# Kernel optimization log

Hardware: AMD Instinct MI355X
Metric: run time of the kernel (lower is better)

Reference implementation:

```python
import jax, jax.numpy as jnp
import numpy as np

# Complete binary tree: node 0 is the root, node i's parent is (i-1)//2.
# adjacency[i, j] = 1 iff j is the parent of i (matches _parent_indices/_child_indices).
N_LEVELS = 11
N_LABELS = 2 ** N_LEVELS - 1  # 2047
N_CLASSES = 2
BATCH = 2048


def _tree_structure():
    # levels[t]: node ids at tree level t (root level 0)
    levels = [np.arange(2 ** t - 1, 2 ** (t + 1) - 1) for t in range(N_LEVELS)]
    parent = np.zeros(N_LABELS, dtype=np.int64)
    parent[1:] = (np.arange(1, N_LABELS) - 1) // 2
    return levels, parent


def _propagate(emissions, transitions, edge_layers):
    """Belief-propagation sweep. edge_layers is a list (per depth, in order)
    of (src, dst) numpy index arrays: each src node sends a message to dst.
    Message: m[b, c_dst, dst] += logsumexp_{c_src}(emissions[b,c_src,src]
              + messages[b,c_src,src] + transitions[dst, src, c_dst, c_src]).
    Identical math to (Batched)MessagePassing.forward, expressed per edge.
    """
    messages = jnp.zeros_like(emissions)
    for src, dst in edge_layers:
        e = emissions[:, :, src] + messages[:, :, src]           # [B, Cs, E]
        t = transitions[dst, src]                                 # [E, Cd, Cs]
        # elem[b, cd, e, cs] = e[b, cs, e] + t[e, cd, cs]
        elem = e.transpose(0, 2, 1)[:, None, :, :] + t.transpose(1, 0, 2)[None]
        contrib = jax.nn.logsumexp(elem, axis=-1)                 # [B, Cd, E]
        messages = messages.at[:, :, dst].add(contrib)
    return messages


def setup_inputs() -> dict:
    key = jax.random.key(0)
    k1, k2 = jax.random.split(key)
    emissions = jax.random.normal(k1, (BATCH, N_CLASSES, N_LABELS), dtype=jnp.float32)
    transitions = jax.random.normal(k2, (N_LABELS, N_LABELS, N_CLASSES, N_CLASSES), dtype=jnp.float32)
    return {"emissions": emissions, "transitions": transitions}


def reference(emissions, transitions):
    levels, parent = _tree_structure()
    # upward (alphas): leaves -> root, successor = parent
    up_edges = [(levels[t], parent[levels[t]]) for t in range(N_LEVELS - 1, 0, -1)]
    # downward (betas): root -> leaves, successor = child
    down_edges = [(parent[levels[t]], levels[t]) for t in range(1, N_LEVELS)]
    alphas = _propagate(emissions, transitions, up_edges)
    betas = _propagate(emissions, transitions, down_edges)
    scores = emissions + alphas + betas                           # [B, C, L]
    # normalize over classes per label -> marginal log-probabilities
    return scores - jax.nn.logsumexp(scores, axis=1, keepdims=True)
```

## Files before the change

kernel.cpp:

```cpp
#include <hip/hip_runtime.h>


#define L 2047
#define NSLOT 49
#define PK_ELEMS (2 * NSLOT * 64)

typedef float __attribute__((ext_vector_type(4), aligned(4))) uf4;
typedef float __attribute__((ext_vector_type(2), aligned(4))) uf2;

__device__ __forceinline__ float lse2(float x, float y) {
    float m = fmaxf(x, y);
    return m + __logf(1.0f + __expf(fminf(x, y) - m));
}

__device__ __forceinline__ void up_pair(float c00, float c01, float c10, float c11,
                                        float4 tA, float4 tB, float em0, float em1,
                                        float& o0, float& o1) {
    o0 = em0 + lse2(c00 + tA.x, c01 + tA.y) + lse2(c10 + tB.x, c11 + tB.y);
    o1 = em1 + lse2(c00 + tA.z, c01 + tA.w) + lse2(c10 + tB.z, c11 + tB.w);
}

__device__ __forceinline__ void slot_decode(int r, int s, int l, int& dst, int& src) {
    const int n7 = 127 + 64 * r + l;
    if (s < 8)       { int k = s >> 1;      dst = 4*n7 + 3 + k;         src = 2*dst + 1 + (s & 1); }
    else if (s < 12) { int j = (s - 8) >> 1;dst = 2*n7 + 1 + j;         src = 2*dst + 1 + (s & 1); }
    else if (s < 14) {                      dst = n7;                   src = 2*n7 + 1 + (s - 12); }
    else if (s < 26) { int d = (s - 14) >> 1; dst = ((n7+1) >> (d+1)) - 1; src = 2*dst + 1 + (s & 1); }
    else if (s < 28) {                      dst = 0;                    src = 1 + (s - 26); }
    else if (s < 34) { int t = s - 27;      dst = ((n7+1) >> (7-t)) - 1; src = (dst - 1) >> 1; }
    else if (s < 35) {                      dst = n7;                   src = (n7 - 1) >> 1; }
    else if (s < 37) {                      dst = 2*n7 + 1 + (s - 35);  src = n7; }
    else if (s < 41) {                      dst = 4*n7 + 3 + (s - 37);  src = (dst - 1) >> 1; }
    else             {                      dst = 8*n7 + 7 + (s - 41);  src = (dst - 1) >> 1; }
}

__global__ void pack_kernel(const float4* __restrict__ tr4, float4* __restrict__ pk) {
    int idx = blockIdx.x * 256 + threadIdx.x;
    if (idx >= PK_ELEMS) return;
    int r = idx / (NSLOT * 64);
    int rem = idx - r * (NSLOT * 64);
    int s = rem >> 6, l = rem & 63;
    int d_, c_; slot_decode(r, s, l, d_, c_);
    pk[idx] = tr4[d_ * L + c_];
}

template <bool UPK>
__global__ __launch_bounds__(128, 4) void treecrf_main(
    const float* __restrict__ emissions,
    const float4* __restrict__ pk,
    const float4* __restrict__ tr4,
    float* __restrict__ out)
{
    __shared__ float sh[4];
    const int tid = threadIdx.x;
    const int l = tid & 63;
    const int r = tid >> 6;
    const int b = blockIdx.x;
    const float* __restrict__ e0 = emissions + (size_t)b * (2 * L);
    const float* __restrict__ e1 = e0 + L;
    float* __restrict__ o0 = out + (size_t)b * (2 * L);
    float* __restrict__ o1 = o0 + L;

    auto FL = [&](int s) -> float4 {
        if (UPK) return pk[((r * NSLOT + s) << 6) + l];
        int d_, c_; slot_decode(r, s, l, d_, c_);
        return tr4[d_ * L + c_];
    };

    float el0[8], el1[8];
    {
        const uf4* p0 = (const uf4*)(e0 + 1023 + 512*r + 8*l);
        const uf4* p1 = (const uf4*)(e1 + 1023 + 512*r + 8*l);
        uf4 a = p0[0], c = p0[1], d = p1[0], e = p1[1];
        el0[0]=a.x; el0[1]=a.y; el0[2]=a.z; el0[3]=a.w;
        el0[4]=c.x; el0[5]=c.y; el0[6]=c.z; el0[7]=c.w;
        el1[0]=d.x; el1[1]=d.y; el1[2]=d.z; el1[3]=d.w;
        el1[4]=e.x; el1[5]=e.y; el1[6]=e.z; el1[7]=e.w;
    }
    float em9_0[4], em9_1[4], em8_0[2], em8_1[2], em7_0, em7_1;
    {
        uf4 a = *(const uf4*)(e0 + 511 + 256*r + 4*l);
        uf4 c = *(const uf4*)(e1 + 511 + 256*r + 4*l);
        em9_0[0]=a.x; em9_0[1]=a.y; em9_0[2]=a.z; em9_0[3]=a.w;
        em9_1[0]=c.x; em9_1[1]=c.y; em9_1[2]=c.z; em9_1[3]=c.w;
        uf2 g = *(const uf2*)(e0 + 255 + 128*r + 2*l);
        uf2 h = *(const uf2*)(e1 + 255 + 128*r + 2*l);
        em8_0[0]=g.x; em8_0[1]=g.y; em8_1[0]=h.x; em8_1[1]=h.y;
        em7_0 = e0[127 + 64*r + l]; em7_1 = e1[127 + 64*r + l];
    }
    float Ea0[7], Ea1[7];
    Ea0[0] = e0[0]; Ea1[0] = e1[0];
    #pragma unroll
    for (int t = 1; t <= 6; ++t) {
        const int n = ((128 + 64*r + l) >> (7 - t)) - 1;
        Ea0[t] = e0[n]; Ea1[t] = e1[n];
    }

    float A9_0[4], A9_1[4];
    #pragma unroll
    for (int k = 0; k < 4; ++k)
        up_pair(el0[2*k], el1[2*k], el0[2*k+1], el1[2*k+1], FL(2*k), FL(2*k+1),
                em9_0[k], em9_1[k], A9_0[k], A9_1[k]);
    float A8_0[2], A8_1[2];
    #pragma unroll
    for (int j = 0; j < 2; ++j)
        up_pair(A9_0[2*j], A9_1[2*j], A9_0[2*j+1], A9_1[2*j+1], FL(8+2*j), FL(9+2*j),
                em8_0[j], em8_1[j], A8_0[j], A8_1[j]);
    float A7_0, A7_1;
    up_pair(A8_0[0], A8_1[0], A8_0[1], A8_1[1], FL(12), FL(13), em7_0, em7_1, A7_0, A7_1);

    float cur0 = A7_0, cur1 = A7_1;
    float Aa0[7], Aa1[7];
    #pragma unroll
    for (int d = 0; d < 6; ++d) {
        const int t = 6 - d;
        float p0v = __shfl_xor(cur0, 1 << d);
        float p1v = __shfl_xor(cur1, 1 << d);
        bool isL = ((l >> d) & 1) == 0;
        float Lc0 = isL ? cur0 : p0v, Lc1 = isL ? cur1 : p1v;
        float Rc0 = isL ? p0v : cur0, Rc1 = isL ? p1v : cur1;
        up_pair(Lc0, Lc1, Rc0, Rc1, FL(14 + 2*d), FL(15 + 2*d),
                Ea0[t], Ea1[t], cur0, cur1);
        Aa0[t] = cur0; Aa1[t] = cur1;
    }

    if (l == 0) { sh[2*r] = cur0; sh[2*r + 1] = cur1; }
    __syncthreads();
    {
        float a1_0 = sh[0], a1_1 = sh[1], a2_0 = sh[2], a2_1 = sh[3];
        float4 t1 = FL(26), t2 = FL(27);
        float AR0 = Ea0[0] + lse2(a1_0 + t1.x, a1_1 + t1.y)
                           + lse2(a2_0 + t2.x, a2_1 + t2.y);
        float AR1 = Ea1[0] + lse2(a1_0 + t1.z, a1_1 + t1.w)
                           + lse2(a2_0 + t2.z, a2_1 + t2.w);
        if (r == 0 && l == 0) {
            float m = lse2(AR0, AR1);
            o0[0] = AR0 - m; o1[0] = AR1 - m;
        }
    }

    float D0 = Ea0[0], D1 = Ea1[0];
    #pragma unroll
    for (int t = 1; t <= 6; ++t) {
        float4 td = FL(27 + t);
        float b0 = lse2(D0 + td.x, D1 + td.y);
        float b1 = lse2(D0 + td.z, D1 + td.w);
        float s0 = Aa0[t] + b0, s1 = Aa1[t] + b1, m = lse2(s0, s1);
        if ((l & ((1 << (7 - t)) - 1)) == 0) {
            const int n = ((128 + 64*r + l) >> (7 - t)) - 1;
            o0[n] = s0 - m; o1[n] = s1 - m;
        }
        D0 = Ea0[t] + b0; D1 = Ea1[t] + b1;
    }

    {
        float4 td = FL(34);
        float b0 = lse2(D0 + td.x, D1 + td.y);
        float b1 = lse2(D0 + td.z, D1 + td.w);
        float s0 = A7_0 + b0, s1 = A7_1 + b1, m = lse2(s0, s1);
        o0[127 + 64*r + l] = s0 - m; o1[127 + 64*r + l] = s1 - m;
        D0 = em7_0 + b0; D1 = em7_1 + b1;
    }

    float D8_0[2], D8_1[2];
    {
        float w0[2], w1[2];
        #pragma unroll
        for (int j = 0; j < 2; ++j) {
            float4 td = FL(35 + j);
            float b0 = lse2(D0 + td.x, D1 + td.y);
            float b1 = lse2(D0 + td.z, D1 + td.w);
            float s0 = A8_0[j] + b0, s1 = A8_1[j] + b1, m = lse2(s0, s1);
            w0[j] = s0 - m; w1[j] = s1 - m;
            D8_0[j] = em8_0[j] + b0; D8_1[j] = em8_1[j] + b1;
        }
        *(uf2*)(o0 + 255 + 128*r + 2*l) = uf2{w0[0], w0[1]};
        *(uf2*)(o1 + 255 + 128*r + 2*l) = uf2{w1[0], w1[1]};
    }

    float D9_0[4], D9_1[4];
    {
        float w0[4], w1[4];
        #pragma unroll
        for (int k = 0; k < 4; ++k) {
            float4 td = FL(37 + k);
            float b0 = lse2(D8_0[k>>1] + td.x, D8_1[k>>1] + td.y);
            float b1 = lse2(D8_0[k>>1] + td.z, D8_1[k>>1] + td.w);
            float s0 = A9_0[k] + b0, s1 = A9_1[k] + b1, m = lse2(s0, s1);
            w0[k] = s0 - m; w1[k] = s1 - m;
            D9_0[k] = em9_0[k] + b0; D9_1[k] = em9_1[k] + b1;
        }
        *(uf4*)(o0 + 511 + 256*r + 4*l) = uf4{w0[0], w0[1], w0[2], w0[3]};
        *(uf4*)(o1 + 511 + 256*r + 4*l) = uf4{w1[0], w1[1], w1[2], w1[3]};
    }

    {
        float w0[8], w1[8];
        #pragma unroll
        for (int m2 = 0; m2 < 8; ++m2) {
            float4 td = FL(41 + m2);
            float b0 = lse2(D9_0[m2>>1] + td.x, D9_1[m2>>1] + td.y);
            float b1 = lse2(D9_0[m2>>1] + td.z, D9_1[m2>>1] + td.w);
            float s0 = el0[m2] + b0, s1 = el1[m2] + b1, m = lse2(s0, s1);
            w0[m2] = s0 - m; w1[m2] = s1 - m;
        }
        uf4* q0 = (uf4*)(o0 + 1023 + 512*r + 8*l);
        uf4* q1 = (uf4*)(o1 + 1023 + 512*r + 8*l);
        q0[0] = uf4{w0[0], w0[1], w0[2], w0[3]}; q0[1] = uf4{w0[4], w0[5], w0[6], w0[7]};
        q1[0] = uf4{w1[0], w1[1], w1[2], w1[3]}; q1[1] = uf4{w1[4], w1[5], w1[6], w1[7]};
    }
}

extern "C" void kernel_launch(void* const* d_in, const int* in_sizes, int n_in,
                              void* d_out, int out_size, void* d_ws, size_t ws_size,
                              hipStream_t stream) {
    const float* emissions = (const float*)d_in[0];
    const float4* tr4 = (const float4*)d_in[1];
    float* out = (float*)d_out;

    const size_t packed_bytes = (size_t)PK_ELEMS * sizeof(float4);
    const bool use_ws = (ws_size >= packed_bytes) && (d_ws != nullptr);
    if (use_ws) {
        float4* pk = (float4*)d_ws;
        pack_kernel<<<(PK_ELEMS + 255) / 256, 256, 0, stream>>>(tr4, pk);
        treecrf_main<true><<<2048, 128, 0, stream>>>(emissions, pk, tr4, out);
    } else {
        treecrf_main<false><<<2048, 128, 0, stream>>>(emissions, nullptr, tr4, out);
    }
}
```

Baseline: 133.5 us.

## Process two batch rows per thread to reuse transition loads

Restructures the main kernel so each thread computes two batch elements, with 256-thread blocks covering four batch rows and a grid of 512 blocks. Each packed transition float4 is loaded once and applied to both rows, halving transition-load traffic per row and adding ILP. The cost is roughly doubled register state per thread, which can reduce occupancy, and fewer, larger blocks.

Result: slower. 136.6 us (+2.3%).

```diff
diff --git a/kernel.cpp b/kernel.cpp
--- a/kernel.cpp
+++ b/kernel.cpp
@@ -45,21 +45,28 @@
 }
 
 template <bool UPK>
-__global__ __launch_bounds__(128, 4) void treecrf_main(
+__global__ __launch_bounds__(256, 2) void treecrf_main(
     const float* __restrict__ emissions,
     const float4* __restrict__ pk,
     const float4* __restrict__ tr4,
     float* __restrict__ out)
 {
-    __shared__ float sh[4];
+    __shared__ float sh[16];
     const int tid = threadIdx.x;
     const int l = tid & 63;
-    const int r = tid >> 6;
-    const int b = blockIdx.x;
-    const float* __restrict__ e0 = emissions + (size_t)b * (2 * L);
-    const float* __restrict__ e1 = e0 + L;
-    float* __restrict__ o0 = out + (size_t)b * (2 * L);
-    float* __restrict__ o1 = o0 + L;
+    const int w = tid >> 6;
+    const int r = w >> 1;
+    const int p = w & 1;
+    const int bb = blockIdx.x * 4 + p * 2;
+
+    const float* e0[2]; const float* e1[2]; float* o0[2]; float* o1[2];
+    #pragma unroll
+    for (int q = 0; q < 2; ++q) {
+        e0[q] = emissions + (size_t)(bb + q) * (2 * L);
+        e1[q] = e0[q] + L;
+        o0[q] = out + (size_t)(bb + q) * (2 * L);
+        o1[q] = o0[q] + L;
+    }
 
     auto FL = [&](int s) -> float4 {
         if (UPK) return pk[((r * NSLOT + s) << 6) + l];
@@ -67,147 +74,201 @@
         return tr4[d_ * L + c_];
     };
 
-    float el0[8], el1[8];
-    {
-        const uf4* p0 = (const uf4*)(e0 + 1023 + 512*r + 8*l);
-        const uf4* p1 = (const uf4*)(e1 + 1023 + 512*r + 8*l);
-        uf4 a = p0[0], c = p0[1], d = p1[0], e = p1[1];
-        el0[0]=a.x; el0[1]=a.y; el0[2]=a.z; el0[3]=a.w;
-        el0[4]=c.x; el0[5]=c.y; el0[6]=c.z; el0[7]=c.w;
-        el1[0]=d.x; el1[1]=d.y; el1[2]=d.z; el1[3]=d.w;
-        el1[4]=e.x; el1[5]=e.y; el1[6]=e.z; el1[7]=e.w;
-    }
-    float em9_0[4], em9_1[4], em8_0[2], em8_1[2], em7_0, em7_1;
-    {
-        uf4 a = *(const uf4*)(e0 + 511 + 256*r + 4*l);
-        uf4 c = *(const uf4*)(e1 + 511 + 256*r + 4*l);
-        em9_0[0]=a.x; em9_0[1]=a.y; em9_0[2]=a.z; em9_0[3]=a.w;
-        em9_1[0]=c.x; em9_1[1]=c.y; em9_1[2]=c.z; em9_1[3]=c.w;
-        uf2 g = *(const uf2*)(e0 + 255 + 128*r + 2*l);
-        uf2 h = *(const uf2*)(e1 + 255 + 128*r + 2*l);
-        em8_0[0]=g.x; em8_0[1]=g.y; em8_1[0]=h.x; em8_1[1]=h.y;
-        em7_0 = e0[127 + 64*r + l]; em7_1 = e1[127 + 64*r + l];
-    }
-    float Ea0[7], Ea1[7];
-    Ea0[0] = e0[0]; Ea1[0] = e1[0];
-    #pragma unroll
-    for (int t = 1; t <= 6; ++t) {
-        const int n = ((128 + 64*r + l) >> (7 - t)) - 1;
-        Ea0[t] = e0[n]; Ea1[t] = e1[n];
-    }
-
-    float A9_0[4], A9_1[4];
-    #pragma unroll
-    for (int k = 0; k < 4; ++k)
-        up_pair(el0[2*k], el1[2*k], el0[2*k+1], el1[2*k+1], FL(2*k), FL(2*k+1),
-                em9_0[k], em9_1[k], A9_0[k], A9_1[k]);
-    float A8_0[2], A8_1[2];
-    #pragma unroll
-    for (int j = 0; j < 2; ++j)
-        up_pair(A9_0[2*j], A9_1[2*j], A9_0[2*j+1], A9_1[2*j+1], FL(8+2*j), FL(9+2*j),
-                em8_0[j], em8_1[j], A8_0[j], A8_1[j]);
-    float A7_0, A7_1;
-    up_pair(A8_0[0], A8_1[0], A8_0[1], A8_1[1], FL(12), FL(13), em7_0, em7_1, A7_0, A7_1);
-
-    float cur0 = A7_0, cur1 = A7_1;
-    float Aa0[7], Aa1[7];
+    float el0[2][8], el1[2][8];
+    float em9_0[2][4], em9_1[2][4], em8_0[2][2], em8_1[2][2], em7_0[2], em7_1[2];
+    float Ea0[2][7], Ea1[2][7];
+    #pragma unroll
+    for (int q = 0; q < 2; ++q) {
+        const uf4* pA = (const uf4*)(e0[q] + 1023 + 512*r + 8*l);
+        const uf4* pB = (const uf4*)(e1[q] + 1023 + 512*r + 8*l);
+        uf4 a = pA[0], b2 = pA[1], c = pB[0], d = pB[1];
+        el0[q][0]=a.x;  el0[q][1]=a.y;  el0[q][2]=a.z;  el0[q][3]=a.w;
+        el0[q][4]=b2.x; el0[q][5]=b2.y; el0[q][6]=b2.z; el0[q][7]=b2.w;
+        el1[q][0]=c.x;  el1[q][1]=c.y;  el1[q][2]=c.z;  el1[q][3]=c.w;
+        el1[q][4]=d.x;  el1[q][5]=d.y;  el1[q][6]=d.z;  el1[q][7]=d.w;
+        uf4 a9 = *(const uf4*)(e0[q] + 511 + 256*r + 4*l);
+        uf4 c9 = *(const uf4*)(e1[q] + 511 + 256*r + 4*l);
+        em9_0[q][0]=a9.x; em9_0[q][1]=a9.y; em9_0[q][2]=a9.z; em9_0[q][3]=a9.w;
+        em9_1[q][0]=c9.x; em9_1[q][1]=c9.y; em9_1[q][2]=c9.z; em9_1[q][3]=c9.w;
+        uf2 g = *(const uf2*)(e0[q] + 255 + 128*r + 2*l);
+        uf2 h = *(const uf2*)(e1[q] + 255 + 128*r + 2*l);
+        em8_0[q][0]=g.x; em8_0[q][1]=g.y; em8_1[q][0]=h.x; em8_1[q][1]=h.y;
+        em7_0[q] = e0[q][127 + 64*r + l]; em7_1[q] = e1[q][127 + 64*r + l];
+        Ea0[q][0] = e0[q][0]; Ea1[q][0] = e1[q][0];
+        #pragma unroll
+        for (int t = 1; t <= 6; ++t) {
+            const int n = ((128 + 64*r + l) >> (7 - t)) - 1;
+            Ea0[q][t] = e0[q][n]; Ea1[q][t] = e1[q][n];
+        }
+    }
+
+    float A9_0[2][4], A9_1[2][4];
+    #pragma unroll
+    for (int k = 0; k < 4; ++k) {
+        float4 tA = FL(2*k), tB = FL(2*k + 1);
+        #pragma unroll
+        for (int q = 0; q < 2; ++q)
+            up_pair(el0[q][2*k], el1[q][2*k], el0[q][2*k+1], el1[q][2*k+1], tA, tB,
+                    em9_0[q][k], em9_1[q][k], A9_0[q][k], A9_1[q][k]);
+    }
+    float A8_0[2][2], A8_1[2][2];
+    #pragma unroll
+    for (int j = 0; j < 2; ++j) {
+        float4 tA = FL(8 + 2*j), tB = FL(9 + 2*j);
+        #pragma unroll
+        for (int q = 0; q < 2; ++q)
+            up_pair(A9_0[q][2*j], A9_1[q][2*j], A9_0[q][2*j+1], A9_1[q][2*j+1], tA, tB,
+                    em8_0[q][j], em8_1[q][j], A8_0[q][j], A8_1[q][j]);
+    }
+    float A7_0[2], A7_1[2];
+    {
+        float4 tA = FL(12), tB = FL(13);
+        #pragma unroll
+        for (int q = 0; q < 2; ++q)
+            up_pair(A8_0[q][0], A8_1[q][0], A8_0[q][1], A8_1[q][1], tA, tB,
+                    em7_0[q], em7_1[q], A7_0[q], A7_1[q]);
+    }
+
+    float cur0[2] = {A7_0[0], A7_0[1]}, cur1[2] = {A7_1[0], A7_1[1]};
+    float Aa0[2][7], Aa1[2][7];
     #pragma unroll
     for (int d = 0; d < 6; ++d) {
         const int t = 6 - d;
-        float p0v = __shfl_xor(cur0, 1 << d);
-        float p1v = __shfl_xor(cur1, 1 << d);
+        float4 tL = FL(14 + 2*d), tR = FL(15 + 2*d);
         bool isL = ((l >> d) & 1) == 0;
-        float Lc0 = isL ? cur0 : p0v, Lc1 = isL ? cur1 : p1v;
-        float Rc0 = isL ? p0v : cur0, Rc1 = isL ? p1v : cur1;
-        up_pair(Lc0, Lc1, Rc0, Rc1, FL(14 + 2*d), FL(15 + 2*d),
-                Ea0[t], Ea1[t], cur0, cur1);
-        Aa0[t] = cur0; Aa1[t] = cur1;
-    }
-
-    if (l == 0) { sh[2*r] = cur0; sh[2*r + 1] = cur1; }
+        #pragma unroll
+        for (int q = 0; q < 2; ++q) {
+            float p0v = __shfl_xor(cur0[q], 1 << d);
+            float p1v = __shfl_xor(cur1[q], 1 << d);
+            float Lc0 = isL ? cur0[q] : p0v, Lc1 = isL ? cur1[q] : p1v;
+            float Rc0 = isL ? p0v : cur0[q], Rc1 = isL ? p1v : cur1[q];
+            up_pair(Lc0, Lc1, Rc0, Rc1, tL, tR, Ea0[q][t], Ea1[q][t],
+                    cur0[q], cur1[q]);
+            Aa0[q][t] = cur0[q]; Aa1[q][t] = cur1[q];
+        }
+    }
+
+    if (l == 0) {
+        #pragma unroll
+        for (int q = 0; q < 2; ++q) {
+            sh[p*8 + q*4 + r*2 + 0] = cur0[q];
+            sh[p*8 + q*4 + r*2 + 1] = cur1[q];
+        }
+    }
     __syncthreads();
     {
-        float a1_0 = sh[0], a1_1 = sh[1], a2_0 = sh[2], a2_1 = sh[3];
         float4 t1 = FL(26), t2 = FL(27);
-        float AR0 = Ea0[0] + lse2(a1_0 + t1.x, a1_1 + t1.y)
-                           + lse2(a2_0 + t2.x, a2_1 + t2.y);
-        float AR1 = Ea1[0] + lse2(a1_0 + t1.z, a1_1 + t1.w)
-                           + lse2(a2_0 + t2.z, a2_1 + t2.w);
         if (r == 0 && l == 0) {
-            float m = lse2(AR0, AR1);
-            o0[0] = AR0 - m; o1[0] = AR1 - m;
-        }
-    }
-
-    float D0 = Ea0[0], D1 = Ea1[0];
+            #pragma unroll
+            for (int q = 0; q < 2; ++q) {
+                float a1_0 = sh[p*8 + q*4 + 0], a1_1 = sh[p*8 + q*4 + 1];
+                float a2_0 = sh[p*8 + q*4 + 2], a2_1 = sh[p*8 + q*4 + 3];
+                float AR0 = Ea0[q][0] + lse2(a1_0 + t1.x, a1_1 + t1.y)
+                                      + lse2(a2_0 + t2.x, a2_1 + t2.y);
+                float AR1 = Ea1[q][0] + lse2(a1_0 + t1.z, a1_1 + t1.w)
+                                      + lse2(a2_0 + t2.z, a2_1 + t2.w);
+                float m = lse2(AR0, AR1);
+                o0[q][0] = AR0 - m; o1[q][0] = AR1 - m;
+            }
+        }
+    }
+
+    float D0[2], D1[2];
+    #pragma unroll
+    for (int q = 0; q < 2; ++q) { D0[q] = Ea0[q][0]; D1[q] = Ea1[q][0]; }
     #pragma unroll
     for (int t = 1; t <= 6; ++t) {
         float4 td = FL(27 + t);
-        float b0 = lse2(D0 + td.x, D1 + td.y);
-        float b1 = lse2(D0 + td.z, D1 + td.w);
-        float s0 = Aa0[t] + b0, s1 = Aa1[t] + b1, m = lse2(s0, s1);
-        if ((l & ((1 << (7 - t)) - 1)) == 0) {
-            const int n = ((128 + 64*r + l) >> (7 - t)) - 1;
-            o0[n] = s0 - m; o1[n] = s1 - m;
-        }
-        D0 = Ea0[t] + b0; D1 = Ea1[t] + b1;
+        const bool emit = (l & ((1 << (7 - t)) - 1)) == 0;
+        const int n = ((128 + 64*r + l) >> (7 - t)) - 1;
+        #pragma unroll
+        for (int q = 0; q < 2; ++q) {
+            float b0v = lse2(D0[q] + td.x, D1[q] + td.y);
+            float b1v = lse2(D0[q] + td.z, D1[q] + td.w);
+            float s0 = Aa0[q][t] + b0v, s1 = Aa1[q][t] + b1v, m = lse2(s0, s1);
+            if (emit) { o0[q][n] = s0 - m; o1[q][n] = s1 - m; }
+            D0[q] = Ea0[q][t] + b0v; D1[q] = Ea1[q][t] + b1v;
+        }
     }
 
     {
         float4 td = FL(34);
-        float b0 = lse2(D0 + td.x, D1 + td.y);
-        float b1 = lse2(D0 + td.z, D1 + td.w);
-        float s0 = A7_0 + b0, s1 = A7_1 + b1, m = lse2(s0, s1);
-        o0[127 + 64*r + l] = s0 - m; o1[127 + 64*r + l] = s1 - m;
-        D0 = em7_0 + b0; D1 = em7_1 + b1;
-    }
-
-    float D8_0[2], D8_1[2];
-    {
-        float w0[2], w1[2];
+        #pragma unroll
+        for (int q = 0; q < 2; ++q) {
+            float b0v = lse2(D0[q] + td.x, D1[q] + td.y);
+            float b1v = lse2(D0[q] + td.z, D1[q] + td.w);
+            float s0 = A7_0[q] + b0v, s1 = A7_1[q] + b1v, m = lse2(s0, s1);
+            o0[q][127 + 64*r + l] = s0 - m; o1[q][127 + 64*r + l] = s1 - m;
+            D0[q] = em7_0[q] + b0v; D1[q] = em7_1[q] + b1v;
+        }
+    }
+
+    float D8_0[2][2], D8_1[2][2];
+    {
+        float w0[2][2], w1[2][2];
         #pragma unroll
         for (int j = 0; j < 2; ++j) {
             float4 td = FL(35 + j);
-            float b0 = lse2(D0 + td.x, D1 + td.y);
-            float b1 = lse2(D0 + td.z, D1 + td.w);
-            float s0 = A8_0[j] + b0, s1 = A8_1[j] + b1, m = lse2(s0, s1);
-            w0[j] = s0 - m; w1[j] = s1 - m;
-            D8_0[j] = em8_0[j] + b0; D8_1[j] = em8_1[j] + b1;
-        }
-        *(uf2*)(o0 + 255 + 128*r + 2*l) = uf2{w0[0], w0[1]};
-        *(uf2*)(o1 + 255 + 128*r + 2*l) = uf2{w1[0], w1[1]};
-    }
-
-    float D9_0[4], D9_1[4];
-    {
-        float w0[4], w1[4];
+            #pragma unroll
+            for (int q = 0; q < 2; ++q) {
+                float b0v = lse2(D0[q] + td.x, D1[q] + td.y);
+                float b1v = lse2(D0[q] + td.z, D1[q] + td.w);
+                float s0 = A8_0[q][j] + b0v, s1 = A8_1[q][j] + b1v, m = lse2(s0, s1);
+                w0[q][j] = s0 - m; w1[q][j] = s1 - m;
+                D8_0[q][j] = em8_0[q][j] + b0v; D8_1[q][j] = em8_1[q][j] + b1v;
+            }
+        }
+        #pragma unroll
+        for (int q = 0; q < 2; ++q) {
+            *(uf2*)(o0[q] + 255 + 128*r + 2*l) = uf2{w0[q][0], w0[q][1]};
+            *(uf2*)(o1[q] + 255 + 128*r + 2*l) = uf2{w1[q][0], w1[q][1]};
+        }
+    }
+
+    float D9_0[2][4], D9_1[2][4];
+    {
+        float w0[2][4], w1[2][4];
         #pragma unroll
         for (int k = 0; k < 4; ++k) {
             float4 td = FL(37 + k);
-            float b0 = lse2(D8_0[k>>1] + td.x, D8_1[k>>1] + td.y);
-            float b1 = lse2(D8_0[k>>1] + td.z, D8_1[k>>1] + td.w);
-            float s0 = A9_0[k] + b0, s1 = A9_1[k] + b1, m = lse2(s0, s1);
-            w0[k] = s0 - m; w1[k] = s1 - m;
-            D9_0[k] = em9_0[k] + b0; D9_1[k] = em9_1[k] + b1;
-        }
-        *(uf4*)(o0 + 511 + 256*r + 4*l) = uf4{w0[0], w0[1], w0[2], w0[3]};
-        *(uf4*)(o1 + 511 + 256*r + 4*l) = uf4{w1[0], w1[1], w1[2], w1[3]};
-    }
-
-    {
-        float w0[8], w1[8];
+            #pragma unroll
+            for (int q = 0; q < 2; ++q) {
+                float b0v = lse2(D8_0[q][k>>1] + td.x, D8_1[q][k>>1] + td.y);
+                float b1v = lse2(D8_0[q][k>>1] + td.z, D8_1[q][k>>1] + td.w);
+                float s0 = A9_0[q][k] + b0v, s1 = A9_1[q][k] + b1v, m = lse2(s0, s1);
+                w0[q][k] = s0 - m; w1[q][k] = s1 - m;
+                D9_0[q][k] = em9_0[q][k] + b0v; D9_1[q][k] = em9_1[q][k] + b1v;
+            }
+        }
+        #pragma unroll
+        for (int q = 0; q < 2; ++q) {
+            *(uf4*)(o0[q] + 511 + 256*r + 4*l) = uf4{w0[q][0], w0[q][1], w0[q][2], w0[q][3]};
+            *(uf4*)(o1[q] + 511 + 256*r + 4*l) = uf4{w1[q][0], w1[q][1], w1[q][2], w1[q][3]};
+        }
+    }
+
+    {
+        float w0[2][8], w1[2][8];
         #pragma unroll
         for (int m2 = 0; m2 < 8; ++m2) {
             float4 td = FL(41 + m2);
-            float b0 = lse2(D9_0[m2>>1] + td.x, D9_1[m2>>1] + td.y);
-            float b1 = lse2(D9_0[m2>>1] + td.z, D9_1[m2>>1] + td.w);
-            float s0 = el0[m2] + b0, s1 = el1[m2] + b1, m = lse2(s0, s1);
-            w0[m2] = s0 - m; w1[m2] = s1 - m;
-        }
-        uf4* q0 = (uf4*)(o0 + 1023 + 512*r + 8*l);
-        uf4* q1 = (uf4*)(o1 + 1023 + 512*r + 8*l);
-        q0[0] = uf4{w0[0], w0[1], w0[2], w0[3]}; q0[1] = uf4{w0[4], w0[5], w0[6], w0[7]};
-        q1[0] = uf4{w1[0], w1[1], w1[2], w1[3]}; q1[1] = uf4{w1[4], w1[5], w1[6], w1[7]};
+            #pragma unroll
+            for (int q = 0; q < 2; ++q) {
+                float b0v = lse2(D9_0[q][m2>>1] + td.x, D9_1[q][m2>>1] + td.y);
+                float b1v = lse2(D9_0[q][m2>>1] + td.z, D9_1[q][m2>>1] + td.w);
+                float s0 = el0[q][m2] + b0v, s1 = el1[q][m2] + b1v, m = lse2(s0, s1);
+                w0[q][m2] = s0 - m; w1[q][m2] = s1 - m;
+            }
+        }
+        #pragma unroll
+        for (int q = 0; q < 2; ++q) {
+            uf4* q0 = (uf4*)(o0[q] + 1023 + 512*r + 8*l);
+            uf4* q1 = (uf4*)(o1[q] + 1023 + 512*r + 8*l);
+            q0[0] = uf4{w0[q][0], w0[q][1], w0[q][2], w0[q][3]};
+            q0[1] = uf4{w0[q][4], w0[q][5], w0[q][6], w0[q][7]};
+            q1[0] = uf4{w1[q][0], w1[q][1], w1[q][2], w1[q][3]};
+            q1[1] = uf4{w1[q][4], w1[q][5], w1[q][6], w1[q][7]};
+        }
     }
 }
 
@@ -223,8 +284,8 @@
     if (use_ws) {
         float4* pk = (float4*)d_ws;
         pack_kernel<<<(PK_ELEMS + 255) / 256, 256, 0, stream>>>(tr4, pk);
-        treecrf_main<true><<<2048, 128, 0, stream>>>(emissions, pk, tr4, out);
+        treecrf_main<true><<<512, 256, 0, stream>>>(emissions, pk, tr4, out);
     } else {
-        treecrf_main<false><<<2048, 128, 0, stream>>>(emissions, nullptr, tr4, out);
-    }
-}
+        treecrf_main<false><<<512, 256, 0, stream>>>(emissions, nullptr, tr4, out);
+    }
+}
```

## Precompute exp of transitions in pack step, use sum-product logsumexp

Applied to the files above, without the earlier changes.

The pack kernel now stores exp(transitions) instead of raw transitions. Upward and downward messages are computed as max plus log of an exp-weighted sum, which cuts the number of exp/log calls per edge (two exps and two logs for a pair instead of four of each). The root computation is also limited to a single thread. This trades some numerical range, since exp(t) is unguarded and products of the sums could under- or overflow, for fewer transcendental instructions.

After: 131.2 us. About the same (-1.7%).

```diff
diff --git a/kernel.cpp b/kernel.cpp
--- a/kernel.cpp
+++ b/kernel.cpp
@@ -13,11 +13,25 @@
     return m + __logf(1.0f + __expf(fminf(x, y) - m));
 }
 
-__device__ __forceinline__ void up_pair(float c00, float c01, float c10, float c11,
-                                        float4 tA, float4 tB, float em0, float em1,
-                                        float& o0, float& o1) {
-    o0 = em0 + lse2(c00 + tA.x, c01 + tA.y) + lse2(c10 + tB.x, c11 + tB.y);
-    o1 = em1 + lse2(c00 + tA.z, c01 + tA.w) + lse2(c10 + tB.z, c11 + tB.w);
+__device__ __forceinline__ void up_pair_e(float c00, float c01, float c10, float c11,
+                                          float4 EA, float4 EB, float em0, float em1,
+                                          float& o0, float& o1) {
+    float mA = fmaxf(c00, c01), mB = fmaxf(c10, c11);
+    float pA0 = __expf(c00 - mA), pA1 = __expf(c01 - mA);
+    float pB0 = __expf(c10 - mB), pB1 = __expf(c11 - mB);
+    float SA0 = pA0 * EA.x + pA1 * EA.y, SA1 = pA0 * EA.z + pA1 * EA.w;
+    float SB0 = pB0 * EB.x + pB1 * EB.y, SB1 = pB0 * EB.z + pB1 * EB.w;
+    float base = mA + mB;
+    o0 = em0 + base + __logf(SA0 * SB0);
+    o1 = em1 + base + __logf(SA1 * SB1);
+}
+
+__device__ __forceinline__ void dn_msg(float D0, float D1, float4 E,
+                                       float& b0, float& b1) {
+    float m = fmaxf(D0, D1);
+    float p0 = __expf(D0 - m), p1 = __expf(D1 - m);
+    b0 = m + __logf(p0 * E.x + p1 * E.y);
+    b1 = m + __logf(p0 * E.z + p1 * E.w);
 }
 
 __device__ __forceinline__ void slot_decode(int r, int s, int l, int& dst, int& src) {
@@ -41,7 +55,8 @@
     int rem = idx - r * (NSLOT * 64);
     int s = rem >> 6, l = rem & 63;
     int d_, c_; slot_decode(r, s, l, d_, c_);
-    pk[idx] = tr4[d_ * L + c_];
+    float4 t = tr4[d_ * L + c_];
+    pk[idx] = float4{__expf(t.x), __expf(t.y), __expf(t.z), __expf(t.w)};
 }
 
 template <bool UPK>
@@ -64,7 +79,8 @@
     auto FL = [&](int s) -> float4 {
         if (UPK) return pk[((r * NSLOT + s) << 6) + l];
         int d_, c_; slot_decode(r, s, l, d_, c_);
-        return tr4[d_ * L + c_];
+        float4 t = tr4[d_ * L + c_];
+        return float4{__expf(t.x), __expf(t.y), __expf(t.z), __expf(t.w)};
     };
 
     float el0[8], el1[8];
@@ -99,15 +115,15 @@
     float A9_0[4], A9_1[4];
     #pragma unroll
     for (int k = 0; k < 4; ++k)
-        up_pair(el0[2*k], el1[2*k], el0[2*k+1], el1[2*k+1], FL(2*k), FL(2*k+1),
-                em9_0[k], em9_1[k], A9_0[k], A9_1[k]);
+        up_pair_e(el0[2*k], el1[2*k], el0[2*k+1], el1[2*k+1], FL(2*k), FL(2*k+1),
+                  em9_0[k], em9_1[k], A9_0[k], A9_1[k]);
     float A8_0[2], A8_1[2];
     #pragma unroll
     for (int j = 0; j < 2; ++j)
-        up_pair(A9_0[2*j], A9_1[2*j], A9_0[2*j+1], A9_1[2*j+1], FL(8+2*j), FL(9+2*j),
-                em8_0[j], em8_1[j], A8_0[j], A8_1[j]);
+        up_pair_e(A9_0[2*j], A9_1[2*j], A9_0[2*j+1], A9_1[2*j+1], FL(8+2*j), FL(9+2*j),
+                  em8_0[j], em8_1[j], A8_0[j], A8_1[j]);
     float A7_0, A7_1;
-    up_pair(A8_0[0], A8_1[0], A8_0[1], A8_1[1], FL(12), FL(13), em7_0, em7_1, A7_0, A7_1);
+    up_pair_e(A8_0[0], A8_1[0], A8_0[1], A8_1[1], FL(12), FL(13), em7_0, em7_1, A7_0, A7_1);
 
     float cur0 = A7_0, cur1 = A7_1;
     float Aa0[7], Aa1[7];
@@ -119,32 +135,26 @@
         bool isL = ((l >> d) & 1) == 0;
         float Lc0 = isL ? cur0 : p0v, Lc1 = isL ? cur1 : p1v;
         float Rc0 = isL ? p0v : cur0, Rc1 = isL ? p1v : cur1;
-        up_pair(Lc0, Lc1, Rc0, Rc1, FL(14 + 2*d), FL(15 + 2*d),
-                Ea0[t], Ea1[t], cur0, cur1);
+        up_pair_e(Lc0, Lc1, Rc0, Rc1, FL(14 + 2*d), FL(15 + 2*d),
+                  Ea0[t], Ea1[t], cur0, cur1);
         Aa0[t] = cur0; Aa1[t] = cur1;
     }
 
     if (l == 0) { sh[2*r] = cur0; sh[2*r + 1] = cur1; }
     __syncthreads();
-    {
-        float a1_0 = sh[0], a1_1 = sh[1], a2_0 = sh[2], a2_1 = sh[3];
-        float4 t1 = FL(26), t2 = FL(27);
-        float AR0 = Ea0[0] + lse2(a1_0 + t1.x, a1_1 + t1.y)
-                           + lse2(a2_0 + t2.x, a2_1 + t2.y);
-        float AR1 = Ea1[0] + lse2(a1_0 + t1.z, a1_1 + t1.w)
-                           + lse2(a2_0 + t2.z, a2_1 + t2.w);
-        if (r == 0 && l == 0) {
-            float m = lse2(AR0, AR1);
-            o0[0] = AR0 - m; o1[0] = AR1 - m;
-        }
+    if (r == 0 && l == 0) {
+        float AR0, AR1;
+        up_pair_e(sh[0], sh[1], sh[2], sh[3], FL(26), FL(27),
+                  Ea0[0], Ea1[0], AR0, AR1);
+        float m = lse2(AR0, AR1);
+        o0[0] = AR0 - m; o1[0] = AR1 - m;
     }
 
     float D0 = Ea0[0], D1 = Ea1[0];
     #pragma unroll
     for (int t = 1; t <= 6; ++t) {
-        float4 td = FL(27 + t);
-        float b0 = lse2(D0 + td.x, D1 + td.y);
-        float b1 = lse2(D0 + td.z, D1 + td.w);
+        float b0, b1;
+        dn_msg(D0, D1, FL(27 + t), b0, b1);
         float s0 = Aa0[t] + b0, s1 = Aa1[t] + b1, m = lse2(s0, s1);
         if ((l & ((1 << (7 - t)) - 1)) == 0) {
             const int n = ((128 + 64*r + l) >> (7 - t)) - 1;
@@ -154,9 +164,8 @@
     }
 
     {
-        float4 td = FL(34);
-        float b0 = lse2(D0 + td.x, D1 + td.y);
-        float b1 = lse2(D0 + td.z, D1 + td.w);
+        float b0, b1;
+        dn_msg(D0, D1, FL(34), b0, b1);
         float s0 = A7_0 + b0, s1 = A7_1 + b1, m = lse2(s0, s1);
         o0[127 + 64*r + l] = s0 - m; o1[127 + 64*r + l] = s1 - m;
         D0 = em7_0 + b0; D1 = em7_1 + b1;
@@ -167,9 +176,8 @@
         float w0[2], w1[2];
         #pragma unroll
         for (int j = 0; j < 2; ++j) {
-            float4 td = FL(35 + j);
-            float b0 = lse2(D0 + td.x, D1 + td.y);
-            float b1 = lse2(D0 + td.z, D1 + td.w);
+            float b0, b1;
+            dn_msg(D0, D1, FL(35 + j), b0, b1);
             float s0 = A8_0[j] + b0, s1 = A8_1[j] + b1, m = lse2(s0, s1);
             w0[j] = s0 - m; w1[j] = s1 - m;
             D8_0[j] = em8_0[j] + b0; D8_1[j] = em8_1[j] + b1;
@@ -183,9 +191,8 @@
         float w0[4], w1[4];
         #pragma unroll
         for (int k = 0; k < 4; ++k) {
-            float4 td = FL(37 + k);
-            float b0 = lse2(D8_0[k>>1] + td.x, D8_1[k>>1] + td.y);
-            float b1 = lse2(D8_0[k>>1] + td.z, D8_1[k>>1] + td.w);
+            float b0, b1;
+            dn_msg(D8_0[k>>1], D8_1[k>>1], FL(37 + k), b0, b1);
             float s0 = A9_0[k] + b0, s1 = A9_1[k] + b1, m = lse2(s0, s1);
             w0[k] = s0 - m; w1[k] = s1 - m;
             D9_0[k] = em9_0[k] + b0; D9_1[k] = em9_1[k] + b1;
@@ -198,9 +205,8 @@
         float w0[8], w1[8];
         #pragma unroll
         for (int m2 = 0; m2 < 8; ++m2) {
-            float4 td = FL(41 + m2);
-            float b0 = lse2(D9_0[m2>>1] + td.x, D9_1[m2>>1] + td.y);
-            float b1 = lse2(D9_0[m2>>1] + td.z, D9_1[m2>>1] + td.w);
+            float b0, b1;
+            dn_msg(D9_0[m2>>1], D9_1[m2>>1], FL(41 + m2), b0, b1);
             float s0 = el0[m2] + b0, s1 = el1[m2] + b1, m = lse2(s0, s1);
             w0[m2] = s0 - m; w1[m2] = s1 - m;
         }
```
